# Kernel optimization log

Measured on AMD Instinct MI355X. Metric: run time of the kernel, lower is better.

## Reference

```python
import jax, jax.numpy as jnp
import numpy as np

HEADS = 8
LANDMARKS = 256
PINV_ITERS = 6
KSZ = 33          # res_conv kernel size (lucidrains default)
LN_EPS = 1e-5


def setup_inputs() -> dict:
    key = jax.random.key(0)
    ks = jax.random.split(key, 5)
    b, n, d = 4, 8192, 512
    inner = 512  # heads * dim_head = 8 * 64
    s = 0.02
    return {
        "x": jax.random.normal(ks[0], (b, n, d), jnp.float32),
        "ln_w": jnp.ones((d,), jnp.float32),
        "ln_b": jnp.zeros((d,), jnp.float32),
        "w_qkv": jax.random.normal(ks[1], (3 * inner, d), jnp.float32) * s,  # Linear(d, 3*inner, bias=False)
        "w_out": jax.random.normal(ks[2], (d, inner), jnp.float32) * s,      # Linear(inner, d)
        "b_out": jnp.zeros((d,), jnp.float32),
        "conv_w": jax.random.normal(ks[3], (HEADS, 1, KSZ, 1), jnp.float32) * 0.1,  # depthwise Conv2d(h,h,(33,1),groups=h)
    }


def _pinv(x, iters):
    # Moore-Penrose iterative pseudo-inverse (lucidrains)
    abs_x = jnp.abs(x)
    scale = jnp.max(abs_x.sum(-1)) * jnp.max(abs_x.sum(-2))
    z = jnp.swapaxes(x, -1, -2) / scale
    I = jnp.eye(x.shape[-1], dtype=x.dtype)
    for _ in range(iters):
        xz = x @ z
        z = 0.25 * z @ (13.0 * I - xz @ (15.0 * I - xz @ (7.0 * I - xz)))
    return z


def _forward(x, ln_w, ln_b, w_qkv, w_out, b_out, conv_w):
    b, n, d = x.shape
    h, m = HEADS, LANDMARKS
    dh = d // h  # 64
    # --- LayerNorm ---
    mu = jnp.mean(x, -1, keepdims=True)
    var = jnp.var(x, -1, keepdims=True)
    xn = (x - mu) / jnp.sqrt(var + LN_EPS) * ln_w + ln_b
    # --- qkv ---
    qkv = xn @ w_qkv.T
    q, k, v = jnp.split(qkv, 3, axis=-1)
    to_heads = lambda t: t.reshape(b, n, h, dh).transpose(0, 2, 1, 3)  # b h n dh
    q = to_heads(q) * (dh ** -0.5)
    k = to_heads(k)
    v = to_heads(v)
    # --- landmarks: mean over contiguous groups of length l (einops '(n l) d -> n d') ---
    l = n // m
    q_l = q.reshape(b, h, m, l, dh).mean(3)  # b h m dh
    k_l = k.reshape(b, h, m, l, dh).mean(3)
    # --- three softmax attention matrices ---
    attn1 = jax.nn.softmax(jnp.einsum('bhid,bhjd->bhij', q, k_l), -1)    # b h n m
    attn2 = jax.nn.softmax(jnp.einsum('bhid,bhjd->bhij', q_l, k_l), -1)  # b h m m
    attn3 = jax.nn.softmax(jnp.einsum('bhid,bhjd->bhij', q_l, k), -1)    # b h m n
    out = (attn1 @ _pinv(attn2, PINV_ITERS)) @ (attn3 @ v)               # b h n dh
    # --- residual depthwise conv over sequence dim, per head, shared over dh ---
    pad = KSZ // 2
    res = jax.lax.conv_general_dilated(
        v, conv_w, window_strides=(1, 1), padding=[(pad, pad), (0, 0)],
        dimension_numbers=('NCHW', 'OIHW', 'NCHW'), feature_group_count=h)
    out = out + res
    out = out.transpose(0, 2, 1, 3).reshape(b, n, h * dh)
    attn_out = out @ w_out.T + b_out  # dropout is identity in eval
    return x + attn_out  # TransLayer residual


def reference(x, ln_w, ln_b, w_qkv, w_out, b_out, conv_w):
    return _forward(x, ln_w, ln_b, w_qkv, w_out, b_out, conv_w)
```

## Files before the change

kernel.cpp:

```cpp
#include <hip/hip_runtime.h>

typedef unsigned short u16;
typedef unsigned int u32;
typedef __attribute__((ext_vector_type(8))) short bf16x8;
typedef __attribute__((ext_vector_type(4))) float f32x4;

__device__ __forceinline__ float bf2f(u16 u) {
    union { u32 i; float f; } z; z.i = ((u32)u) << 16; return z.f;
}
__device__ __forceinline__ float bflo(u32 w) {
    union { u32 i; float f; } z; z.i = w << 16; return z.f;
}
__device__ __forceinline__ float bfhi(u32 w) {
    union { u32 i; float f; } z; z.i = w & 0xffff0000u; return z.f;
}
__device__ __forceinline__ u16 f2bf(float f) {
    union { float f; u32 i; } z; z.f = f;
    u32 x = z.i;
    return (u16)((x + 0x7FFFu + ((x >> 16) & 1u)) >> 16);
}
__device__ __forceinline__ u32 pack2bf(float a, float b) {
    return (u32)f2bf(a) | ((u32)f2bf(b) << 16);
}
template<int BF>
__device__ __forceinline__ float ldin(const void* p, size_t i) {
    return BF ? bf2f(((const u16*)p)[i]) : ((const float*)p)[i];
}


__global__ void detect_dtype(const void* lnw, int* flg) {
    if (threadIdx.x == 0 && blockIdx.x == 0) {
        u32 w = *(const u32*)lnw;
        *flg = (w == 0x3F803F80u) ? 1 : 0;
    }
}

__global__ __launch_bounds__(256) void conv2bf(const void* src, u16* dst, int count, const int* flg) {
    int idx = (blockIdx.x * 256 + threadIdx.x) * 4;
    if (idx >= count) return;
    if (*flg) {
        *(ulonglong1*)&dst[idx] = *(const ulonglong1*)&((const u16*)src)[idx];
    } else {
        const float* s = (const float*)src;
        u32 p0 = pack2bf(s[idx], s[idx + 1]);
        u32 p1 = pack2bf(s[idx + 2], s[idx + 3]);
        *(uint2*)&dst[idx] = make_uint2(p0, p1);
    }
}

template<int BF>
__device__ void ln_fused_body(const void* x, const void* lnw, const void* lnb,
                              u16* xn, float* s1, float* s2) {
    int r = blockIdx.x, t = threadIdx.x;
    size_t base = (size_t)r * 512;
    float a = ldin<BF>(x, base + 2 * t);
    float b = ldin<BF>(x, base + 2 * t + 1);
    s1[t] = a + b; s2[t] = a * a + b * b;
    __syncthreads();
    for (int off = 128; off; off >>= 1) {
        if (t < off) { s1[t] += s1[t + off]; s2[t] += s2[t + off]; }
        __syncthreads();
    }
    float mu = s1[0] * (1.f / 512.f);
    float var = s2[0] * (1.f / 512.f) - mu * mu;
    float rstd = rsqrtf(var + 1e-5f);
    float w0 = ldin<BF>(lnw, 2 * t), w1 = ldin<BF>(lnw, 2 * t + 1);
    float b0 = ldin<BF>(lnb, 2 * t), b1 = ldin<BF>(lnb, 2 * t + 1);
    float v0 = (a - mu) * rstd * w0 + b0;
    float v1 = (b - mu) * rstd * w1 + b1;
    ((u32*)(xn + base))[t] = pack2bf(v0, v1);
}
__global__ __launch_bounds__(256) void ln_fused(
    const void* x, const void* lnw, const void* lnb, u16* xn, const int* flg) {
    __shared__ float s1[256], s2[256];
    if (*flg) ln_fused_body<1>(x, lnw, lnb, xn, s1, s2);
    else      ln_fused_body<0>(x, lnw, lnb, xn, s1, s2);
}

__global__ __launch_bounds__(256) void mfma_gemm_qkv(
    const u16* __restrict__ A, const u16* __restrict__ B,
    u16* __restrict__ qp, u16* __restrict__ kp, u16* __restrict__ vp)
{
    __shared__ u16 Asl[128][40];
    __shared__ u16 Bsl[128][40];
    int t = threadIdx.x;
    int wave = t >> 6, lane = t & 63;
    int bid = blockIdx.y * 12 + blockIdx.x;
    int w = (bid & 7) * 384 + (bid >> 3);
    int col0 = (w % 12) * 128, row0 = (w / 12) * 128;
    int wr = (wave & 1) * 64, wc = (wave >> 1) * 64;
    int lrow = lane & 15, koff = (lane >> 4) * 8;
    f32x4 acc[4][4] = {};
    int srow = t >> 2, sch = (t & 3) * 8;
    for (int k0 = 0; k0 < 512; k0 += 32) {
        *(float4*)&Asl[srow][sch]      = *(const float4*)&A[(size_t)(row0 + srow) * 512 + k0 + sch];
        *(float4*)&Asl[srow + 64][sch] = *(const float4*)&A[(size_t)(row0 + srow + 64) * 512 + k0 + sch];
        *(float4*)&Bsl[srow][sch]      = *(const float4*)&B[(size_t)(col0 + srow) * 512 + k0 + sch];
        *(float4*)&Bsl[srow + 64][sch] = *(const float4*)&B[(size_t)(col0 + srow + 64) * 512 + k0 + sch];
        __syncthreads();
        bf16x8 af[4], bfr[4];
#pragma unroll
        for (int i = 0; i < 4; i++) af[i]  = *(const bf16x8*)&Asl[wr + 16 * i + lrow][koff];
#pragma unroll
        for (int j = 0; j < 4; j++) bfr[j] = *(const bf16x8*)&Bsl[wc + 16 * j + lrow][koff];
#pragma unroll
        for (int i = 0; i < 4; i++)
#pragma unroll
            for (int j = 0; j < 4; j++)
                acc[i][j] = __builtin_amdgcn_mfma_f32_16x16x32_bf16(af[i], bfr[j], acc[i][j], 0, 0, 0);
        __syncthreads();
    }
    int crow = (lane >> 4) * 4, ccol = lane & 15;
#pragma unroll
    for (int i = 0; i < 4; i++) {
#pragma unroll
        for (int j = 0; j < 4; j++) {
#pragma unroll
            for (int rg = 0; rg < 4; rg++) {
                int row = row0 + wr + 16 * i + crow + rg;
                int col = col0 + wc + 16 * j + ccol;
                int bi = row >> 13, ii = row & 8191;
                int which = col >> 9, wi = col & 511, hh = wi >> 6, cc = wi & 63;
                size_t dst = (((size_t)bi * 8 + hh) * 8192 + ii) * 64 + cc;
                float v = acc[i][j][rg];
                if (which == 0)      qp[dst] = f2bf(v * 0.125f);
                else if (which == 1) kp[dst] = f2bf(v);
                else                 vp[dst] = f2bf(v);
            }
        }
    }
}

__global__ __launch_bounds__(256) void landmark_kernel(
    const u16* __restrict__ q, const u16* __restrict__ k,
    float* __restrict__ q_l, float* __restrict__ k_l,
    u16* __restrict__ q_l_bf, u16* __restrict__ k_l_bf)
{
    int bh = blockIdx.x;
    int g = blockIdx.y * 4 + (threadIdx.x >> 6);
    int c = threadIdx.x & 63;
    const u16* src = blockIdx.z ? k : q;
    float* dst = blockIdx.z ? k_l : q_l;
    u16* dstbf = blockIdx.z ? k_l_bf : q_l_bf;
    const u16* p0 = src + (((size_t)bh * 8192) + (size_t)g * 32) * 64 + c;
    float s = 0.f;
#pragma unroll
    for (int il = 0; il < 32; il++) s += bf2f(p0[(size_t)il * 64]);
    float mean = s * (1.f / 32.f);
    dst[((size_t)bh * 256 + g) * 64 + c] = mean;
    dstbf[((size_t)bh * 256 + g) * 64 + c] = f2bf(mean);
}

__global__ __launch_bounds__(256) void attn2_kernel(
    const float* __restrict__ q_l, const float* __restrict__ k_l, float* __restrict__ attn2)
{
    int bh = blockIdx.x, i = blockIdx.y, j = threadIdx.x;
    __shared__ float qrow[64];
    __shared__ float red[256];
    if (j < 64) qrow[j] = q_l[((size_t)bh * 256 + i) * 64 + j];
    __syncthreads();
    const float* kb = k_l + ((size_t)bh * 256 + j) * 64;
    float s = 0.f;
#pragma unroll
    for (int c = 0; c < 64; c++) s += qrow[c] * kb[c];
    red[j] = s; __syncthreads();
    for (int off = 128; off; off >>= 1) { if (j < off) red[j] = fmaxf(red[j], red[j + off]); __syncthreads(); }
    float mx = red[0]; __syncthreads();
    float e = __expf(s - mx);
    red[j] = e; __syncthreads();
    for (int off = 128; off; off >>= 1) { if (j < off) red[j] += red[j + off]; __syncthreads(); }
    attn2[((size_t)bh * 256 + i) * 256 + j] = e / red[0];
}

__global__ void init_scale(float* s) { if (threadIdx.x < 2) s[threadIdx.x] = 0.f; }

__global__ __launch_bounds__(256) void colrow_max(const float* __restrict__ X, float* __restrict__ scl)
{
    int bh = blockIdx.x, t = threadIdx.x;
    const float* Xb = X + (size_t)bh * 65536;
    float cs = 0.f, rs = 0.f;
    for (int i = 0; i < 256; i++) cs += fabsf(Xb[(size_t)i * 256 + t]);
    for (int j = 0; j < 256; j++) rs += fabsf(Xb[(size_t)t * 256 + j]);
    __shared__ float red[256];
    red[t] = cs; __syncthreads();
    for (int off = 128; off; off >>= 1) { if (t < off) red[t] = fmaxf(red[t], red[t + off]); __syncthreads(); }
    float cmax = red[0]; __syncthreads();
    red[t] = rs; __syncthreads();
    for (int off = 128; off; off >>= 1) { if (t < off) red[t] = fmaxf(red[t], red[t + off]); __syncthreads(); }
    if (t == 0) {
        atomicMax((u32*)&scl[0], __float_as_uint(red[0]));
        atomicMax((u32*)&scl[1], __float_as_uint(cmax));
    }
}

__global__ __launch_bounds__(256) void zinit_p(
    const float* __restrict__ X, const float* __restrict__ scl,
    u16* __restrict__ Zh, u16* __restrict__ Zl)
{
    int b = blockIdx.x, i = blockIdx.y, j = threadIdx.x;
    float s = scl[0] * scl[1];
    float v = X[((size_t)b * 256 + j) * 256 + i] / s;
    u16 hi = f2bf(v);
    u16 lo = f2bf(v - bf2f(hi));
    size_t idx = ((size_t)b * 256 + i) * 256 + j;
    Zh[idx] = hi; Zl[idx] = lo;
}

__global__ __launch_bounds__(256) void split_at2(
    const float* __restrict__ src, u16* __restrict__ dh, u16* __restrict__ dl)
{
    int idx = (blockIdx.x * 256 + threadIdx.x) * 4;
    float4 v = *(const float4*)&src[idx];
    ushort4 h, l;
    h.x = f2bf(v.x); l.x = f2bf(v.x - bf2f(h.x));
    h.y = f2bf(v.y); l.y = f2bf(v.y - bf2f(h.y));
    h.z = f2bf(v.z); l.z = f2bf(v.z - bf2f(h.z));
    h.w = f2bf(v.w); l.w = f2bf(v.w - bf2f(h.w));
    *(ushort4*)&dh[idx] = h;
    *(ushort4*)&dl[idx] = l;
}

__global__ __launch_bounds__(256) void bmm_fused(
    const float* __restrict__ A, const float* __restrict__ B,
    float* __restrict__ C, float* __restrict__ Cneg,
    int N, float alpha, float cdiag)
{
    int batch = blockIdx.x;
    int row0 = blockIdx.y * 64, col0 = blockIdx.z * 64;
    const float* Ab = A + (size_t)batch * 256 * 256;
    const float* Bb = B + (size_t)batch * 256 * N;
    __shared__ float As[32][68];
    __shared__ float Bs[32][68];
    int t = threadIdx.x, tx = t & 15, ty = t >> 4;
    float acc[4][4] = {};
    for (int k0 = 0; k0 < 256; k0 += 32) {
#pragma unroll
        for (int p = 0; p < 8; p++) {
            int idx = t + 256 * p;
            int ra = idx >> 5, ca = idx & 31;
            As[ca][ra] = Ab[(size_t)(row0 + ra) * 256 + k0 + ca];
            int kb = idx >> 6, cb = idx & 63;
            Bs[kb][cb] = Bb[(size_t)(k0 + kb) * N + col0 + cb];
        }
        __syncthreads();
#pragma unroll
        for (int kk = 0; kk < 32; kk++) {
            float4 av = *(const float4*)&As[kk][ty * 4];
            float4 bv = *(const float4*)&Bs[kk][tx * 4];
            float a[4] = {av.x, av.y, av.z, av.w};
            float bb[4] = {bv.x, bv.y, bv.z, bv.w};
#pragma unroll
            for (int i = 0; i < 4; i++)
#pragma unroll
                for (int j = 0; j < 4; j++) acc[i][j] += a[i] * bb[j];
        }
        __syncthreads();
    }
#pragma unroll
    for (int i = 0; i < 4; i++) {
        int row = row0 + ty * 4 + i;
#pragma unroll
        for (int j = 0; j < 4; j++) {
            int col = col0 + tx * 4 + j;
            float v = alpha * acc[i][j];
            size_t idx = (size_t)batch * 256 * N + (size_t)row * N + col;
            if (C)    C[idx] = v;
            if (Cneg) Cneg[idx] = ((row == col) ? cdiag : 0.f) - v;
        }
    }
}

__global__ __launch_bounds__(256) void bmm3p(
    const u16* __restrict__ Ahg, const u16* __restrict__ Alg,
    const u16* __restrict__ Bhg, const u16* __restrict__ Blg,
    u16* __restrict__ Ch, u16* __restrict__ Cl,
    u16* __restrict__ Nh, u16* __restrict__ Nl,
    float* __restrict__ Cf, float alpha, float cdiag)
{
    __shared__ u16 Ah[64][40], Al[64][40], Bh[64][40], Bl[64][40];
    int batch = blockIdx.x;
    int row0 = blockIdx.y * 64, col0 = blockIdx.z * 64;
    size_t boff = (size_t)batch * 65536;
    int t = threadIdx.x, wave = t >> 6, lane = t & 63;
    int lrow = lane & 15, koff = (lane >> 4) * 8;
    int ar = t >> 2, akq = (t & 3) * 8;
    f32x4 acc[4] = {};
    for (int k0 = 0; k0 < 256; k0 += 32) {
        *(uint4*)&Ah[ar][akq] = *(const uint4*)&Ahg[boff + (size_t)(row0 + ar) * 256 + k0 + akq];
        *(uint4*)&Al[ar][akq] = *(const uint4*)&Alg[boff + (size_t)(row0 + ar) * 256 + k0 + akq];
#pragma unroll
        for (int p = 0; p < 2; p++) {
            int c = t + 256 * p; int n = c & 63, kq = (c >> 6) * 4;
            size_t bb = boff + (size_t)(k0 + kq) * 256 + col0 + n;
            ushort4 hv, lv;
            hv.x = Bhg[bb];       lv.x = Blg[bb];
            hv.y = Bhg[bb + 256]; lv.y = Blg[bb + 256];
            hv.z = Bhg[bb + 512]; lv.z = Blg[bb + 512];
            hv.w = Bhg[bb + 768]; lv.w = Blg[bb + 768];
            *(ushort4*)&Bh[n][kq] = hv;
            *(ushort4*)&Bl[n][kq] = lv;
        }
        __syncthreads();
        bf16x8 ah = *(const bf16x8*)&Ah[wave * 16 + lrow][koff];
        bf16x8 al = *(const bf16x8*)&Al[wave * 16 + lrow][koff];
#pragma unroll
        for (int j = 0; j < 4; j++) {
            bf16x8 bhv = *(const bf16x8*)&Bh[16 * j + lrow][koff];
            bf16x8 blv = *(const bf16x8*)&Bl[16 * j + lrow][koff];
            acc[j] = __builtin_amdgcn_mfma_f32_16x16x32_bf16(ah, bhv, acc[j], 0, 0, 0);
            acc[j] = __builtin_amdgcn_mfma_f32_16x16x32_bf16(ah, blv, acc[j], 0, 0, 0);
            acc[j] = __builtin_amdgcn_mfma_f32_16x16x32_bf16(al, bhv, acc[j], 0, 0, 0);
        }
        __syncthreads();
    }
    int crow = (lane >> 4) * 4, ccol = lane & 15;
#pragma unroll
    for (int j = 0; j < 4; j++) {
#pragma unroll
        for (int r = 0; r < 4; r++) {
            int row = row0 + wave * 16 + crow + r;
            int col = col0 + 16 * j + ccol;
            float v = alpha * acc[j][r];
            size_t idx = boff + (size_t)row * 256 + col;
            if (Cf) Cf[idx] = v;
            if (Ch) {
                u16 hi = f2bf(v);
                Ch[idx] = hi; Cl[idx] = f2bf(v - bf2f(hi));
            }
            if (Nh) {
                float w = ((row == col) ? cdiag : 0.f) - v;
                u16 hi = f2bf(w);
                Nh[idx] = hi; Nl[idx] = f2bf(w - bf2f(hi));
            }
        }
    }
}

__global__ __launch_bounds__(256) void t2bf(const float* __restrict__ src, u16* __restrict__ dst)
{
    __shared__ u16 tile[256][72];
    int bh = blockIdx.x, t = threadIdx.x;
    const float* s = src + (size_t)bh * 16384;
    u16* d = dst + (size_t)bh * 16384;
#pragma unroll
    for (int p = 0; p < 64; p++) {
        int idx = t + 256 * p;
        tile[idx >> 6][idx & 63] = f2bf(s[idx]);
    }
    __syncthreads();
#pragma unroll
    for (int p = 0; p < 64; p++) {
        int o = t + 256 * p;
        int n = o >> 8, kk = o & 255;
        d[o] = tile[kk][n];
    }
}

__global__ __launch_bounds__(256) void attn3v_mfma(
    const u16* __restrict__ qlbf, const u16* __restrict__ k, const u16* __restrict__ v,
    float* __restrict__ Opart, float* __restrict__ lpart)
{
    __shared__ __align__(16) char smem[8192 + 8192 + 9216];
    char* QsB = smem;
    char* KsB = smem + 8192;
    char* VtB = smem + 16384;

    int bh = blockIdx.x, rb = blockIdx.y, seg = blockIdx.z;
    int t = threadIdx.x;
    int w = t >> 6, lane = t & 63, cl = lane & 15, kg = lane >> 4;
    int wrow = w * 16;

    {
        const uint4* qg = (const uint4*)(qlbf + ((size_t)bh * 256 + rb * 64) * 64);
#pragma unroll
        for (int p = 0; p < 2; p++) {
            int c = t + 256 * p; int row = c >> 3, cc = c & 7;
            *(uint4*)(QsB + row * 128 + ((cc * 16) ^ ((row & 7) << 4))) = qg[c];
        }
    }
    __syncthreads();
    bf16x8 af0, af1;
    {
        int row = wrow + cl, sw = (row & 7) << 4;
        af0 = *(const bf16x8*)(QsB + row * 128 + ((kg * 16) ^ sw));
        af1 = *(const bf16x8*)(QsB + row * 128 + ((kg * 16 + 64) ^ sw));
    }

    const uint4* kb4 = (const uint4*)(k + (size_t)bh * 8192 * 64);
    const uint4* vb4 = (const uint4*)(v + (size_t)bh * 8192 * 64);

    int krow = t >> 3, kcc = t & 7;
    int pn = t >> 3, vcc = t & 7;

    f32x4 acc_o[4] = {};
    float rsum[4] = {0.f, 0.f, 0.f, 0.f};

    int n0 = seg * 2048;
    uint4 kr0 = kb4[(size_t)(n0 + krow) * 8 + kcc];
    uint4 kr1 = kb4[(size_t)(n0 + krow + 32) * 8 + kcc];
    uint4 va  = vb4[(size_t)(n0 + 2 * pn) * 8 + vcc];
    uint4 vbv = vb4[(size_t)(n0 + 2 * pn + 1) * 8 + vcc];

    for (int ti = 0; ti < 32; ti++) {
        __syncthreads();
        *(uint4*)(KsB + krow * 128 + ((kcc * 16) ^ ((krow & 7) << 4))) = kr0;
        {
            int row = krow + 32;
            *(uint4*)(KsB + row * 128 + ((kcc * 16) ^ ((row & 7) << 4))) = kr1;
        }
        {
            u32 aw[4] = {va.x, va.y, va.z, va.w};
            u32 bw[4] = {vbv.x, vbv.y, vbv.z, vbv.w};
            int colb = pn * 4;
#pragma unroll
            for (int e = 0; e < 8; e++) {
                u32 avv = (aw[e >> 1] >> ((e & 1) * 16)) & 0xffffu;
                u32 bvv = (bw[e >> 1] >> ((e & 1) * 16)) & 0xffffu;
                int row = vcc * 8 + e;
                *(u32*)(VtB + row * 144 + (colb ^ ((row & 0x38) << 1))) = avv | (bvv << 16);
            }
        }
        __syncthreads();
        if (ti < 31) {
            int nn = n0 + (ti + 1) * 64;
            kr0 = kb4[(size_t)(nn + krow) * 8 + kcc];
            kr1 = kb4[(size_t)(nn + krow + 32) * 8 + kcc];
            va  = vb4[(size_t)(nn + 2 * pn) * 8 + vcc];
            vbv = vb4[(size_t)(nn + 2 * pn + 1) * 8 + vcc];
        }
        f32x4 s[4] = {};
#pragma unroll
        for (int j = 0; j < 4; j++) {
            int row = 16 * j + cl, sw = (row & 7) << 4;
            bf16x8 b0 = *(const bf16x8*)(KsB + row * 128 + ((kg * 16) ^ sw));
            bf16x8 b1 = *(const bf16x8*)(KsB + row * 128 + ((kg * 16 + 64) ^ sw));
            s[j] = __builtin_amdgcn_mfma_f32_16x16x32_bf16(af0, b0, s[j], 0, 0, 0);
            s[j] = __builtin_amdgcn_mfma_f32_16x16x32_bf16(af1, b1, s[j], 0, 0, 0);
        }
#pragma unroll
        for (int j = 0; j < 4; j++)
#pragma unroll
            for (int r = 0; r < 4; r++) {
                float e = __expf(s[j][r]);
                s[j][r] = e;
                rsum[r] += e;
            }
#pragma unroll
        for (int j = 0; j < 4; j++) {
#pragma unroll
            for (int r = 0; r < 4; r++) {
                float pv = s[j][r];
                float po = __shfl_xor(pv, 1);
                if (!(cl & 1)) {
                    int row = wrow + kg * 4 + r;
                    int col = 16 * j + cl;
                    *(u32*)(QsB + row * 128 + ((col * 2) ^ ((row & 7) << 4))) = pack2bf(pv, po);
                }
            }
        }
        {
            int prow = wrow + cl, psw = (prow & 7) << 4;
            bf16x8 pa0 = *(const bf16x8*)(QsB + prow * 128 + ((kg * 16) ^ psw));
            bf16x8 pa1 = *(const bf16x8*)(QsB + prow * 128 + ((kg * 16 + 64) ^ psw));
#pragma unroll
            for (int j = 0; j < 4; j++) {
                int vr = 16 * j + cl;
                int vsw = (vr & 0x38) << 1;
                bf16x8 vb0 = *(const bf16x8*)(VtB + vr * 144 + ((kg * 16) ^ vsw));
                bf16x8 vb1 = *(const bf16x8*)(VtB + vr * 144 + ((kg * 16 + 64) ^ vsw));
                acc_o[j] = __builtin_amdgcn_mfma_f32_16x16x32_bf16(pa0, vb0, acc_o[j], 0, 0, 0);
                acc_o[j] = __builtin_amdgcn_mfma_f32_16x16x32_bf16(pa1, vb1, acc_o[j], 0, 0, 0);
            }
        }
    }
#pragma unroll
    for (int j = 0; j < 4; j++)
#pragma unroll
        for (int r = 0; r < 4; r++) {
            int lm = rb * 64 + wrow + kg * 4 + r;
            Opart[(((size_t)(bh * 256 + lm)) * 4 + seg) * 64 + 16 * j + cl] = acc_o[j][r];
        }
#pragma unroll
    for (int m = 1; m < 16; m <<= 1)
#pragma unroll
        for (int r = 0; r < 4; r++) rsum[r] += __shfl_xor(rsum[r], m);
    if (cl == 0) {
#pragma unroll
        for (int r = 0; r < 4; r++)
            lpart[((size_t)(bh * 256 + rb * 64 + wrow + kg * 4 + r)) * 4 + seg] = rsum[r];
    }
}

__global__ __launch_bounds__(256) void merge3(
    const float* __restrict__ Opart, const float* __restrict__ lpart, float* __restrict__ w3v)
{
    size_t idx = (size_t)blockIdx.x * 256 + threadIdx.x;
    size_t row = idx >> 6; int c = (int)(idx & 63);
    float l = lpart[row * 4] + lpart[row * 4 + 1] + lpart[row * 4 + 2] + lpart[row * 4 + 3];
    float ov = 0.f;
#pragma unroll
    for (int s = 0; s < 4; s++) ov += Opart[(row * 4 + s) * 64 + c];
    w3v[idx] = ov / l;
}

__global__ __launch_bounds__(256) void attn1_out_mfma(
    const u16* __restrict__ q, const u16* __restrict__ klbf,
    const u16* __restrict__ tmatT, const u16* __restrict__ v,
    const void* __restrict__ conv_w, u16* __restrict__ out2, const int* flg)
{
    __shared__ __align__(16) char smem[8192 * 3 + 13824];
    char* QsB = smem;
    char* KsB = smem + 8192;
    char* TsB = smem + 16384;
    char* VsB = smem + 24576;
    float* Osm = (float*)smem;
    __shared__ float cw[33];

    int bh = blockIdx.x, rb = blockIdx.y;
    int bi = bh >> 3, h = bh & 7;
    int r0 = rb * 64;
    int t = threadIdx.x;
    int w = t >> 6, lane = t & 63, cl = lane & 15, kg = lane >> 4;
    int wrow = w * 16;

    {
        const uint4* qg = (const uint4*)(q + ((size_t)bh * 8192 + r0) * 64);
#pragma unroll
        for (int p = 0; p < 2; p++) {
            int c = t + 256 * p; int row = c >> 3, cc = c & 7;
            *(uint4*)(QsB + row * 128 + ((cc * 16) ^ ((row & 7) << 4))) = qg[c];
        }
        const uint4* vg = (const uint4*)(v + (size_t)bh * 8192 * 64);
#pragma unroll
        for (int p = 0; p < 3; p++) {
            int c = t + 256 * p; int vr = c >> 3, cc = c & 7;
            int gr = r0 - 16 + vr;
            uint4 vv = (gr >= 0 && gr < 8192) ? vg[(size_t)gr * 8 + cc] : make_uint4(0, 0, 0, 0);
            *(uint4*)(VsB + vr * 144 + cc * 16) = vv;
        }
    }
    if (t < 33) cw[t] = (*flg) ? bf2f(((const u16*)conv_w)[h * 33 + t])
                               : ((const float*)conv_w)[h * 33 + t];
    __syncthreads();

    bf16x8 af0, af1;
    {
        int row = wrow + cl, sw = (row & 7) << 4;
        af0 = *(const bf16x8*)(QsB + row * 128 + ((kg * 16) ^ sw));
        af1 = *(const bf16x8*)(QsB + row * 128 + ((kg * 16 + 64) ^ sw));
    }

    const uint4* klg = (const uint4*)(klbf + (size_t)bh * 16384);
    const uint4* tg  = (const uint4*)(tmatT + (size_t)bh * 16384);

    f32x4 accO[4] = {};
    float rsum[4] = {0.f, 0.f, 0.f, 0.f};

    for (int lc = 0; lc < 4; lc++) {
        __syncthreads();
#pragma unroll
        for (int p = 0; p < 2; p++) {
            int c = t + 256 * p; int row = c >> 3, cc = c & 7;
            *(uint4*)(KsB + row * 128 + ((cc * 16) ^ ((row & 7) << 4))) = klg[(size_t)(lc * 64 + row) * 8 + cc];
        }
#pragma unroll
        for (int p = 0; p < 2; p++) {
            int c = t + 256 * p; int n = c >> 3, cc = c & 7;
            *(uint4*)(TsB + n * 128 + ((cc * 16) ^ ((n & 7) << 4))) = tg[(size_t)n * 32 + lc * 8 + cc];
        }
        __syncthreads();
        f32x4 s[4] = {};
#pragma unroll
        for (int j = 0; j < 4; j++) {
            int row = 16 * j + cl, sw = (row & 7) << 4;
            bf16x8 b0 = *(const bf16x8*)(KsB + row * 128 + ((kg * 16) ^ sw));
            bf16x8 b1 = *(const bf16x8*)(KsB + row * 128 + ((kg * 16 + 64) ^ sw));
            s[j] = __builtin_amdgcn_mfma_f32_16x16x32_bf16(af0, b0, s[j], 0, 0, 0);
            s[j] = __builtin_amdgcn_mfma_f32_16x16x32_bf16(af1, b1, s[j], 0, 0, 0);
        }
#pragma unroll
        for (int j = 0; j < 4; j++)
#pragma unroll
            for (int r = 0; r < 4; r++) {
                float e = __expf(s[j][r]);
                s[j][r] = e;
                rsum[r] += e;
            }
#pragma unroll
        for (int j = 0; j < 4; j++) {
#pragma unroll
            for (int r = 0; r < 4; r++) {
                float pv = s[j][r];
                float po = __shfl_xor(pv, 1);
                if (!(cl & 1)) {
                    int row = wrow + kg * 4 + r;
                    int col = 16 * j + cl;
                    *(u32*)(QsB + row * 128 + ((col * 2) ^ ((row & 7) << 4))) = pack2bf(pv, po);
                }
            }
        }
        {
            int prow = wrow + cl, psw = (prow & 7) << 4;
            bf16x8 pa0 = *(const bf16x8*)(QsB + prow * 128 + ((kg * 16) ^ psw));
            bf16x8 pa1 = *(const bf16x8*)(QsB + prow * 128 + ((kg * 16 + 64) ^ psw));
#pragma unroll
            for (int j = 0; j < 4; j++) {
                int n = 16 * j + cl, tsw = (n & 7) << 4;
                bf16x8 b0 = *(const bf16x8*)(TsB + n * 128 + ((kg * 16) ^ tsw));
                bf16x8 b1 = *(const bf16x8*)(TsB + n * 128 + ((kg * 16 + 64) ^ tsw));
                accO[j] = __builtin_amdgcn_mfma_f32_16x16x32_bf16(pa0, b0, accO[j], 0, 0, 0);
                accO[j] = __builtin_amdgcn_mfma_f32_16x16x32_bf16(pa1, b1, accO[j], 0, 0, 0);
            }
        }
    }
#pragma unroll
    for (int m = 1; m < 16; m <<= 1)
#pragma unroll
        for (int r = 0; r < 4; r++) rsum[r] += __shfl_xor(rsum[r], m);
    float linv[4];
#pragma unroll
    for (int r = 0; r < 4; r++) linv[r] = 1.f / rsum[r];
#pragma unroll
    for (int j = 0; j < 4; j++)
#pragma unroll
        for (int r = 0; r < 4; r++) accO[j][r] *= linv[r];

    __syncthreads();
#pragma unroll
    for (int j = 0; j < 4; j++)
#pragma unroll
        for (int r = 0; r < 4; r++)
            Osm[(wrow + kg * 4 + r) * 64 + 16 * j + cl] = accO[j][r];
    __syncthreads();
    float cwr[33];
#pragma unroll
    for (int i = 0; i < 33; i++) cwr[i] = cw[i];
    int rgrp = t >> 4, cchunk = t & 15;
    float racc[4][4] = {};
#pragma unroll
    for (int vri = 0; vri < 36; vri++) {
        int vr = rgrp * 4 + vri;
        uint2 vv = *(const uint2*)(VsB + vr * 144 + cchunk * 8);
        float v0 = bflo(vv.x), v1 = bfhi(vv.x), v2 = bflo(vv.y), v3 = bfhi(vv.y);
#pragma unroll
        for (int rr = 0; rr < 4; rr++) {
            int tap = vri - rr;
            if (tap >= 0 && tap < 33) {
                float cwt = cwr[tap];
                racc[rr][0] += cwt * v0;
                racc[rr][1] += cwt * v1;
                racc[rr][2] += cwt * v2;
                racc[rr][3] += cwt * v3;
            }
        }
    }
#pragma unroll
    for (int rr = 0; rr < 4; rr++) {
        int ro = rgrp * 4 + rr;
        float4 ov = *(const float4*)&Osm[ro * 64 + cchunk * 4];
        float f0 = ov.x + racc[rr][0];
        float f1 = ov.y + racc[rr][1];
        float f2 = ov.z + racc[rr][2];
        float f3 = ov.w + racc[rr][3];
        size_t base = ((size_t)bi * 8192 + r0 + ro) * 512 + h * 64 + cchunk * 4;
        *(uint2*)(out2 + base) = make_uint2(pack2bf(f0, f1), pack2bf(f2, f3));
    }
}

__global__ __launch_bounds__(256) void mfma_gemm_out(
    const u16* __restrict__ A, const u16* __restrict__ B,
    const void* __restrict__ bias, const void* __restrict__ x,
    void* __restrict__ out, const int* flg)
{
    __shared__ u16 Asl[128][40];
    __shared__ u16 Bsl[128][40];
    int t = threadIdx.x;
    int wave = t >> 6, lane = t & 63;
    int bid = blockIdx.y * 4 + blockIdx.x;
    int w = (bid & 7) * 128 + (bid >> 3);
    int col0 = (w & 3) * 128, row0 = (w >> 2) * 128;
    int wr = (wave & 1) * 64, wc = (wave >> 1) * 64;
    int lrow = lane & 15, koff = (lane >> 4) * 8;
    f32x4 acc[4][4] = {};
    int srow = t >> 2, sch = (t & 3) * 8;
    for (int k0 = 0; k0 < 512; k0 += 32) {
        *(float4*)&Asl[srow][sch]      = *(const float4*)&A[(size_t)(row0 + srow) * 512 + k0 + sch];
        *(float4*)&Asl[srow + 64][sch] = *(const float4*)&A[(size_t)(row0 + srow + 64) * 512 + k0 + sch];
        *(float4*)&Bsl[srow][sch]      = *(const float4*)&B[(size_t)(col0 + srow) * 512 + k0 + sch];
        *(float4*)&Bsl[srow + 64][sch] = *(const float4*)&B[(size_t)(col0 + srow + 64) * 512 + k0 + sch];
        __syncthreads();
        bf16x8 af[4], bfr[4];
#pragma unroll
        for (int i = 0; i < 4; i++) af[i]  = *(const bf16x8*)&Asl[wr + 16 * i + lrow][koff];
#pragma unroll
        for (int j = 0; j < 4; j++) bfr[j] = *(const bf16x8*)&Bsl[wc + 16 * j + lrow][koff];
#pragma unroll
        for (int i = 0; i < 4; i++)
#pragma unroll
            for (int j = 0; j < 4; j++)
                acc[i][j] = __builtin_amdgcn_mfma_f32_16x16x32_bf16(af[i], bfr[j], acc[i][j], 0, 0, 0);
        __syncthreads();
    }
    int crow = (lane >> 4) * 4, ccol = lane & 15;
    int isbf = *flg;
#pragma unroll
    for (int i = 0; i < 4; i++) {
#pragma unroll
        for (int j = 0; j < 4; j++) {
#pragma unroll
            for (int rg = 0; rg < 4; rg++) {
                int row = row0 + wr + 16 * i + crow + rg;
                int col = col0 + wc + 16 * j + ccol;
                size_t idx = (size_t)row * 512 + col;
                float bv = isbf ? bf2f(((const u16*)bias)[col]) : ((const float*)bias)[col];
                float xv = isbf ? bf2f(((const u16*)x)[idx]) : ((const float*)x)[idx];
                float v = acc[i][j][rg] + bv + xv;
                if (isbf) ((u16*)out)[idx] = f2bf(v);
                else      ((float*)out)[idx] = v;
            }
        }
    }
}

extern "C" void kernel_launch(void* const* d_in, const int* in_sizes, int n_in,
                              void* d_out, int out_size, void* d_ws, size_t ws_size,
                              hipStream_t stream) {
    const void* x      = d_in[0];
    const void* ln_w   = d_in[1];
    const void* ln_b   = d_in[2];
    const void* w_qkv  = d_in[3];
    const void* w_out  = d_in[4];
    const void* b_out  = d_in[5];
    const void* conv_w = d_in[6];

    char* base = (char*)d_ws;
    size_t off = 0;
    auto alloc = [&](size_t nbytes) { char* p = base + off; off += (nbytes + 255) & ~size_t(255); return p; };
    u16*   q_bf  = (u16*)  alloc(16777216ull * 2);
    u16*   k_bf  = (u16*)  alloc(16777216ull * 2);
    u16*   v_bf  = (u16*)  alloc(16777216ull * 2);
    u16*   xn_bf = (u16*)  alloc(16777216ull * 2);
    u16*   wq_bf = (u16*)  alloc(786432ull * 2);
    u16*   wo_bf = (u16*)  alloc(262144ull * 2);
    float* q_l   = (float*)alloc(524288ull * 4);
    float* k_l   = (float*)alloc(524288ull * 4);
    float* at2   = (float*)alloc(2097152ull * 4);
    float* zf32  = (float*)alloc(2097152ull * 4);
    float* Zb    = (float*)alloc(2097152ull * 4);
    float* XZ    = (float*)alloc(2097152ull * 4);
    u16*   T1h   = (u16*)  alloc(2097152ull * 2);
    u16*   T1l   = (u16*)  alloc(2097152ull * 2);
    float* w3v   = (float*)alloc(524288ull * 4);
    float* tmat  = (float*)alloc(524288ull * 4);
    u16*   ql_bf = (u16*)  alloc(524288ull * 2);
    u16*   kl_bf = (u16*)  alloc(524288ull * 2);
    u16*   tmT   = (u16*)  alloc(524288ull * 2);
    float* scl   = (float*)alloc(256);
    int*   flg   = (int*)  alloc(256);

    u16* a2h = xn_bf;
    u16* a2l = xn_bf + 2097152ull;
    u16* Zah = xn_bf + 2097152ull * 2;
    u16* Zal = xn_bf + 2097152ull * 3;
    u16* Zbh = xn_bf + 2097152ull * 4;
    u16* Zbl = xn_bf + 2097152ull * 5;
    u16* XZh = xn_bf + 2097152ull * 6;
    u16* XZl = xn_bf + 2097152ull * 7;

    detect_dtype<<<1, 64, 0, stream>>>(ln_w, flg);
    ln_fused<<<32768, 256, 0, stream>>>(x, ln_w, ln_b, xn_bf, flg);
    conv2bf<<<768, 256, 0, stream>>>(w_qkv, wq_bf, 786432, flg);
    conv2bf<<<256, 256, 0, stream>>>(w_out, wo_bf, 262144, flg);
    mfma_gemm_qkv<<<dim3(12, 256), 256, 0, stream>>>(xn_bf, wq_bf, q_bf, k_bf, v_bf);
    landmark_kernel<<<dim3(32, 64, 2), 256, 0, stream>>>(q_bf, k_bf, q_l, k_l, ql_bf, kl_bf);
    attn2_kernel<<<dim3(32, 256), 256, 0, stream>>>(q_l, k_l, at2);
    init_scale<<<1, 64, 0, stream>>>(scl);
    colrow_max<<<32, 256, 0, stream>>>(at2, scl);
    zinit_p<<<dim3(32, 256), 256, 0, stream>>>(at2, scl, Zah, Zal);
    split_at2<<<2048, 256, 0, stream>>>(at2, a2h, a2l);

    u16 *zch = Zah, *zcl = Zal, *znh = Zbh, *znl = Zbl;
    for (int it = 0; it < 6; it++) {
        bmm3p<<<dim3(32, 4, 4), 256, 0, stream>>>(a2h, a2l, zch, zcl, XZh, XZl, T1h, T1l, nullptr, 1.f, 7.f);
        bmm3p<<<dim3(32, 4, 4), 256, 0, stream>>>(XZh, XZl, T1h, T1l, nullptr, nullptr, znh, znl, nullptr, 1.f, 15.f);
        bmm3p<<<dim3(32, 4, 4), 256, 0, stream>>>(XZh, XZl, znh, znl, nullptr, nullptr, T1h, T1l, nullptr, 1.f, 13.f);
        bmm3p<<<dim3(32, 4, 4), 256, 0, stream>>>(zch, zcl, T1h, T1l, znh, znl, nullptr, nullptr,
                                                  (it == 5) ? zf32 : nullptr, 0.25f, 0.f);
        u16* th = zch; zch = znh; znh = th;
        u16* tl = zcl; zcl = znl; znl = tl;
    }
    float* Opart = Zb;
    float* lpart = XZ;

    attn3v_mfma<<<dim3(32, 4, 4), 256, 0, stream>>>(ql_bf, k_bf, v_bf, Opart, lpart);
    merge3<<<2048, 256, 0, stream>>>(Opart, lpart, w3v);
    bmm_fused<<<dim3(32, 4, 1), 256, 0, stream>>>(zf32, w3v, tmat, nullptr, 64, 1.f, 0.f);
    t2bf<<<32, 256, 0, stream>>>(tmat, tmT);
    u16* out2 = k_bf;
    attn1_out_mfma<<<dim3(32, 128), 256, 0, stream>>>(q_bf, kl_bf, tmT, v_bf, conv_w, out2, flg);
    mfma_gemm_out<<<dim3(4, 256), 256, 0, stream>>>(out2, wo_bf, b_out, x, d_out, flg);
}
```

Baseline: 902.5 us.

## Rewrite LayerNorm per-wave, transpose Z-init via smem, skip row-sum scan

LayerNorm now processes one row per wave with vector loads and shuffle reductions, replacing the shared-memory tree reduction and using a quarter as many blocks. The pinv scale drops the row-sum pass and fixes the row max at 1.0, relying on softmax rows summing to one. zinit now transposes through a padded shared tile for coalesced reads. In attn1_out the V halo load is moved after the main loop into registers, and the O staging buffer is padded to avoid bank conflicts, shrinking shared memory.

New measurement: 868.4 us. 1.04x faster.

```diff
diff --git a/kernel.cpp b/kernel.cpp
--- a/kernel.cpp
+++ b/kernel.cpp
@@ -49,32 +49,65 @@
 }
 
 template<int BF>
-__device__ void ln_fused_body(const void* x, const void* lnw, const void* lnb,
-                              u16* xn, float* s1, float* s2) {
-    int r = blockIdx.x, t = threadIdx.x;
-    size_t base = (size_t)r * 512;
-    float a = ldin<BF>(x, base + 2 * t);
-    float b = ldin<BF>(x, base + 2 * t + 1);
-    s1[t] = a + b; s2[t] = a * a + b * b;
-    __syncthreads();
-    for (int off = 128; off; off >>= 1) {
-        if (t < off) { s1[t] += s1[t + off]; s2[t] += s2[t + off]; }
-        __syncthreads();
-    }
-    float mu = s1[0] * (1.f / 512.f);
-    float var = s2[0] * (1.f / 512.f) - mu * mu;
+__device__ __forceinline__ void ln_row(const void* x, const void* lnw, const void* lnb, u16* xn) {
+    int lane = threadIdx.x & 63;
+    size_t row = (size_t)blockIdx.x * 4 + (threadIdx.x >> 6);
+    size_t base = row * 512;
+    float v[8];
+    if (BF) {
+        uint4 u = ((const uint4*)((const u16*)x + base))[lane];
+        u32 wd[4] = {u.x, u.y, u.z, u.w};
+#pragma unroll
+        for (int e = 0; e < 4; e++) { v[2 * e] = bflo(wd[e]); v[2 * e + 1] = bfhi(wd[e]); }
+    } else {
+        const float4* xp = (const float4*)((const float*)x + base) + 2 * lane;
+        float4 a = xp[0], b = xp[1];
+        v[0] = a.x; v[1] = a.y; v[2] = a.z; v[3] = a.w;
+        v[4] = b.x; v[5] = b.y; v[6] = b.z; v[7] = b.w;
+    }
+    float s = 0.f, s2 = 0.f;
+#pragma unroll
+    for (int e = 0; e < 8; e++) { s += v[e]; s2 += v[e] * v[e]; }
+#pragma unroll
+    for (int m = 1; m < 64; m <<= 1) { s += __shfl_xor(s, m); s2 += __shfl_xor(s2, m); }
+    float mu = s * (1.f / 512.f);
+    float var = s2 * (1.f / 512.f) - mu * mu;
     float rstd = rsqrtf(var + 1e-5f);
-    float w0 = ldin<BF>(lnw, 2 * t), w1 = ldin<BF>(lnw, 2 * t + 1);
-    float b0 = ldin<BF>(lnb, 2 * t), b1 = ldin<BF>(lnb, 2 * t + 1);
-    float v0 = (a - mu) * rstd * w0 + b0;
-    float v1 = (b - mu) * rstd * w1 + b1;
-    ((u32*)(xn + base))[t] = pack2bf(v0, v1);
+    float wv[8], bv[8];
+    if (BF) {
+        uint4 uw = ((const uint4*)lnw)[lane];
+        uint4 ub = ((const uint4*)lnb)[lane];
+        u32 ww[4] = {uw.x, uw.y, uw.z, uw.w};
+        u32 bb[4] = {ub.x, ub.y, ub.z, ub.w};
+#pragma unroll
+        for (int e = 0; e < 4; e++) {
+            wv[2 * e] = bflo(ww[e]); wv[2 * e + 1] = bfhi(ww[e]);
+            bv[2 * e] = bflo(bb[e]); bv[2 * e + 1] = bfhi(bb[e]);
+        }
+    } else {
+        const float4* wp = (const float4*)lnw + 2 * lane;
+        const float4* bp = (const float4*)lnb + 2 * lane;
+        float4 w0 = wp[0], w1 = wp[1], b0 = bp[0], b1 = bp[1];
+        wv[0] = w0.x; wv[1] = w0.y; wv[2] = w0.z; wv[3] = w0.w;
+        wv[4] = w1.x; wv[5] = w1.y; wv[6] = w1.z; wv[7] = w1.w;
+        bv[0] = b0.x; bv[1] = b0.y; bv[2] = b0.z; bv[3] = b0.w;
+        bv[4] = b1.x; bv[5] = b1.y; bv[6] = b1.z; bv[7] = b1.w;
+    }
+    uint4 o;
+    u32 ow[4];
+#pragma unroll
+    for (int e = 0; e < 4; e++) {
+        float f0 = (v[2 * e] - mu) * rstd * wv[2 * e] + bv[2 * e];
+        float f1 = (v[2 * e + 1] - mu) * rstd * wv[2 * e + 1] + bv[2 * e + 1];
+        ow[e] = pack2bf(f0, f1);
+    }
+    o.x = ow[0]; o.y = ow[1]; o.z = ow[2]; o.w = ow[3];
+    ((uint4*)(xn + base))[lane] = o;
 }
 __global__ __launch_bounds__(256) void ln_fused(
     const void* x, const void* lnw, const void* lnb, u16* xn, const int* flg) {
-    __shared__ float s1[256], s2[256];
-    if (*flg) ln_fused_body<1>(x, lnw, lnb, xn, s1, s2);
-    else      ln_fused_body<0>(x, lnw, lnb, xn, s1, s2);
+    if (*flg) ln_row<1>(x, lnw, lnb, xn);
+    else      ln_row<0>(x, lnw, lnb, xn);
 }
 
 __global__ __launch_bounds__(256) void mfma_gemm_qkv(
@@ -172,38 +205,47 @@
     attn2[((size_t)bh * 256 + i) * 256 + j] = e / red[0];
 }
 
-__global__ void init_scale(float* s) { if (threadIdx.x < 2) s[threadIdx.x] = 0.f; }
-
-__global__ __launch_bounds__(256) void colrow_max(const float* __restrict__ X, float* __restrict__ scl)
+__global__ void init_scale(float* s) {
+    if (threadIdx.x == 0) { s[0] = 1.0f; s[1] = 0.f; }
+}
+
+__global__ __launch_bounds__(256) void colmax_kernel(const float* __restrict__ X, float* __restrict__ scl)
 {
     int bh = blockIdx.x, t = threadIdx.x;
     const float* Xb = X + (size_t)bh * 65536;
-    float cs = 0.f, rs = 0.f;
+    float cs = 0.f;
     for (int i = 0; i < 256; i++) cs += fabsf(Xb[(size_t)i * 256 + t]);
-    for (int j = 0; j < 256; j++) rs += fabsf(Xb[(size_t)t * 256 + j]);
     __shared__ float red[256];
     red[t] = cs; __syncthreads();
     for (int off = 128; off; off >>= 1) { if (t < off) red[t] = fmaxf(red[t], red[t + off]); __syncthreads(); }
-    float cmax = red[0]; __syncthreads();
-    red[t] = rs; __syncthreads();
-    for (int off = 128; off; off >>= 1) { if (t < off) red[t] = fmaxf(red[t], red[t + off]); __syncthreads(); }
-    if (t == 0) {
-        atomicMax((u32*)&scl[0], __float_as_uint(red[0]));
-        atomicMax((u32*)&scl[1], __float_as_uint(cmax));
-    }
+    if (t == 0) atomicMax((u32*)&scl[1], __float_as_uint(red[0]));
 }
 
 __global__ __launch_bounds__(256) void zinit_p(
     const float* __restrict__ X, const float* __restrict__ scl,
     u16* __restrict__ Zh, u16* __restrict__ Zl)
 {
-    int b = blockIdx.x, i = blockIdx.y, j = threadIdx.x;
+    __shared__ float tile[64][65];
+    int b = blockIdx.x;
+    int j0 = blockIdx.y * 64, i0 = blockIdx.z * 64;
     float s = scl[0] * scl[1];
-    float v = X[((size_t)b * 256 + j) * 256 + i] / s;
-    u16 hi = f2bf(v);
-    u16 lo = f2bf(v - bf2f(hi));
-    size_t idx = ((size_t)b * 256 + i) * 256 + j;
-    Zh[idx] = hi; Zl[idx] = lo;
+    const float* Xb = X + (size_t)b * 65536;
+    int t = threadIdx.x;
+#pragma unroll
+    for (int p = 0; p < 16; p++) {
+        int idx = t + 256 * p; int jj = idx >> 6, ii = idx & 63;
+        tile[jj][ii] = Xb[(size_t)(j0 + jj) * 256 + i0 + ii];
+    }
+    __syncthreads();
+#pragma unroll
+    for (int p = 0; p < 16; p++) {
+        int idx = t + 256 * p; int ii = idx >> 6, jj = idx & 63;
+        float v = tile[jj][ii] / s;
+        u16 hi = f2bf(v);
+        u16 lo = f2bf(v - bf2f(hi));
+        size_t o = ((size_t)b * 256 + i0 + ii) * 256 + j0 + jj;
+        Zh[o] = hi; Zl[o] = lo;
+    }
 }
 
 __global__ __launch_bounds__(256) void split_at2(
@@ -508,12 +550,12 @@
     const u16* __restrict__ tmatT, const u16* __restrict__ v,
     const void* __restrict__ conv_w, u16* __restrict__ out2, const int* flg)
 {
-    __shared__ __align__(16) char smem[8192 * 3 + 13824];
+    __shared__ __align__(16) char smem[31296];
     char* QsB = smem;
     char* KsB = smem + 8192;
     char* TsB = smem + 16384;
-    char* VsB = smem + 24576;
     float* Osm = (float*)smem;
+    char* VsB = smem + 17472;
     __shared__ float cw[33];
 
     int bh = blockIdx.x, rb = blockIdx.y;
@@ -529,14 +571,6 @@
         for (int p = 0; p < 2; p++) {
             int c = t + 256 * p; int row = c >> 3, cc = c & 7;
             *(uint4*)(QsB + row * 128 + ((cc * 16) ^ ((row & 7) << 4))) = qg[c];
-        }
-        const uint4* vg = (const uint4*)(v + (size_t)bh * 8192 * 64);
-#pragma unroll
-        for (int p = 0; p < 3; p++) {
-            int c = t + 256 * p; int vr = c >> 3, cc = c & 7;
-            int gr = r0 - 16 + vr;
-            uint4 vv = (gr >= 0 && gr < 8192) ? vg[(size_t)gr * 8 + cc] : make_uint4(0, 0, 0, 0);
-            *(uint4*)(VsB + vr * 144 + cc * 16) = vv;
         }
     }
     if (t < 33) cw[t] = (*flg) ? bf2f(((const u16*)conv_w)[h * 33 + t])
@@ -626,11 +660,26 @@
         for (int r = 0; r < 4; r++) accO[j][r] *= linv[r];
 
     __syncthreads();
+    uint4 vreg[3];
+    {
+        const uint4* vg = (const uint4*)(v + (size_t)bh * 8192 * 64);
+#pragma unroll
+        for (int p = 0; p < 3; p++) {
+            int c = t + 256 * p; int vr = c >> 3, cc = c & 7;
+            int gr = r0 - 16 + vr;
+            vreg[p] = (gr >= 0 && gr < 8192) ? vg[(size_t)gr * 8 + cc] : make_uint4(0, 0, 0, 0);
+        }
+    }
 #pragma unroll
     for (int j = 0; j < 4; j++)
 #pragma unroll
         for (int r = 0; r < 4; r++)
-            Osm[(wrow + kg * 4 + r) * 64 + 16 * j + cl] = accO[j][r];
+            Osm[(wrow + kg * 4 + r) * 68 + 16 * j + cl] = accO[j][r];
+#pragma unroll
+    for (int p = 0; p < 3; p++) {
+        int c = t + 256 * p; int vr = c >> 3, cc = c & 7;
+        *(uint4*)(VsB + vr * 144 + cc * 16) = vreg[p];
+    }
     __syncthreads();
     float cwr[33];
 #pragma unroll
@@ -657,7 +706,7 @@
 #pragma unroll
     for (int rr = 0; rr < 4; rr++) {
         int ro = rgrp * 4 + rr;
-        float4 ov = *(const float4*)&Osm[ro * 64 + cchunk * 4];
+        float4 ov = *(const float4*)&Osm[ro * 68 + cchunk * 4];
         float f0 = ov.x + racc[rr][0];
         float f1 = ov.y + racc[rr][1];
         float f2 = ov.z + racc[rr][2];
@@ -768,15 +817,15 @@
     u16* XZl = xn_bf + 2097152ull * 7;
 
     detect_dtype<<<1, 64, 0, stream>>>(ln_w, flg);
-    ln_fused<<<32768, 256, 0, stream>>>(x, ln_w, ln_b, xn_bf, flg);
+    ln_fused<<<8192, 256, 0, stream>>>(x, ln_w, ln_b, xn_bf, flg);
     conv2bf<<<768, 256, 0, stream>>>(w_qkv, wq_bf, 786432, flg);
     conv2bf<<<256, 256, 0, stream>>>(w_out, wo_bf, 262144, flg);
     mfma_gemm_qkv<<<dim3(12, 256), 256, 0, stream>>>(xn_bf, wq_bf, q_bf, k_bf, v_bf);
     landmark_kernel<<<dim3(32, 64, 2), 256, 0, stream>>>(q_bf, k_bf, q_l, k_l, ql_bf, kl_bf);
     attn2_kernel<<<dim3(32, 256), 256, 0, stream>>>(q_l, k_l, at2);
     init_scale<<<1, 64, 0, stream>>>(scl);
-    colrow_max<<<32, 256, 0, stream>>>(at2, scl);
-    zinit_p<<<dim3(32, 256), 256, 0, stream>>>(at2, scl, Zah, Zal);
+    colmax_kernel<<<32, 256, 0, stream>>>(at2, scl);
+    zinit_p<<<dim3(32, 4, 4), 256, 0, stream>>>(at2, scl, Zah, Zal);
     split_at2<<<2048, 256, 0, stream>>>(at2, a2h, a2l);
 
     u16 *zch = Zah, *zcl = Zal, *znh = Zbh, *znl = Zbl;
```
